# Performance work log

Measured on AMD Instinct MI355X. Metric: run time of the kernel, lower is better.

Reference implementation:

```python
import jax, jax.numpy as jnp
import numpy as np

EPS = 1e-6
INV_T = 1.0
STEPS = 6  # TRAIN_STEPS (module defaults to training mode)
NORM_EPS = 1e-12  # F.normalize default eps


def _l2norm_dim1(t):
    # F.normalize(t, p=2, dim=1): divide by clamped L2 norm over feature dim D
    n = jnp.sqrt(jnp.sum(t * t, axis=1, keepdims=True))
    return t / jnp.maximum(n, NORM_EPS)


def setup_inputs() -> dict:
    key = jax.random.key(0)
    k1, k2 = jax.random.split(key)
    x5d = jax.random.normal(k1, (2, 512, 16, 64, 64), dtype=jnp.float32)
    bases = jax.random.uniform(k2, (2, 512, 64), dtype=jnp.float32)  # (B*S, D_feat, R)
    return {"x5d": x5d, "bases": bases}


def reference(x5d, bases):
    B, C, Dv, H, W = x5d.shape
    S = 1
    D_feat = C // S
    N = Dv * H * W
    x = x5d.reshape(B * S, D_feat, N)  # (BS, D, N)

    b = _l2norm_dim1(bases)  # _build_bases normalizes over D
    # coef init uses UNCLAMPED x (clamp happens in-place only inside local_step)
    coef = jax.nn.softmax(INV_T * jnp.einsum('bdn,bdr->bnr', x, b), axis=-1)

    xc = jnp.maximum(x, EPS)  # clamp_input_nonneg, applied in-place on first MU step

    def mu_step(carry, _):
        b, c = carry
        BtB = jnp.einsum('bdr,bds->brs', b, b)            # (BS,R,R)
        numC = jnp.einsum('bdn,bdr->bnr', xc, b)          # (BS,N,R)
        denC = jnp.einsum('bnr,brs->bns', c, BtB) + EPS
        c = c * numC / denC
        CtC = jnp.einsum('bnr,bns->brs', c, c)            # (BS,R,R)
        numB = jnp.einsum('bdn,bnr->bdr', xc, c)          # (BS,D,R)
        denB = jnp.einsum('bdr,brs->bds', b, CtC) + EPS
        b = b * numB / denB
        b = jnp.maximum(b, EPS)
        c = jnp.maximum(c, EPS)
        b = _l2norm_dim1(b)  # normalize_each_step
        return (b, c), None

    (b, coef), _ = jax.lax.scan(mu_step, (b, coef), None, length=STEPS)

    # compute_coef (differentiable refinement in the original)
    BtB = jnp.einsum('bdr,bds->brs', b, b)
    numC = jnp.einsum('bdn,bdr->bnr', xc, b)
    denC = jnp.einsum('bnr,brs->bns', coef, BtB) + EPS
    c_new = coef * (numC / denC)

    x_hat = jnp.einsum('bdr,bnr->bdn', b, c_new)  # (BS, D, N)
    return x_hat.reshape(B, C, Dv, H, W)
```

## Files before the change

### kernel.cpp

```cpp
#include <hip/hip_runtime.h>
#include <math.h>

#define DD   512
#define NTOT 65536
#define RR   64
#define NB   2
#define EPSV 1e-6f

typedef unsigned short u16;
typedef __attribute__((ext_vector_type(8))) short bf16x8;
typedef __attribute__((ext_vector_type(8))) unsigned short us8;
typedef __attribute__((ext_vector_type(4))) unsigned short us4;
typedef __attribute__((ext_vector_type(4))) float f32x4;

__device__ inline u16 f2bf(float f) {
    union { float f; unsigned u; } x; x.f = f;
    unsigned r = x.u + 0x7FFFu + ((x.u >> 16) & 1u);
    return (u16)(r >> 16);
}
__device__ inline float bf2f(u16 h) {
    union { unsigned u; float f; } x; x.u = ((unsigned)h) << 16;
    return x.f;
}
__device__ inline u16 clamp1(u16 h) {
    short t = (short)h;
    return (u16)(t < (short)0x3586 ? (short)0x3586 : t);
}

#define MFMA16(a, b, c) __builtin_amdgcn_mfma_f32_16x16x32_bf16((a), (b), (c), 0, 0, 0)

__global__ __launch_bounds__(256) void convert_x_kernel(const float* __restrict__ x,
                                                        u16* __restrict__ xd,
                                                        u16* __restrict__ xTr,
                                                        u16* __restrict__ xTc) {
    int s = blockIdx.z, d0 = blockIdx.y * 64, n0 = blockIdx.x * 64;
    const float* xp = x + ((size_t)s * DD + d0) * NTOT + n0;
    u16* xdp = xd + ((size_t)s * DD + d0) * NTOT + n0;
    u16* xtr = xTr + ((size_t)s * NTOT + n0) * DD + d0;
    u16* xtc = xTc + ((size_t)s * NTOT + n0) * DD + d0;
    __shared__ u16 L[64][66];
    int tid = threadIdx.x;
#pragma unroll
    for (int k = 0; k < 4; ++k) {
        int f4 = tid + k * 256;
        int dr = f4 >> 4, c4 = (f4 & 15) * 4;
        float4 v = *(const float4*)&xp[(size_t)dr * NTOT + c4];
        u16 h0 = f2bf(v.x), h1 = f2bf(v.y), h2 = f2bf(v.z), h3 = f2bf(v.w);
        xdp[(size_t)dr * NTOT + c4 + 0] = clamp1(h0);
        xdp[(size_t)dr * NTOT + c4 + 1] = clamp1(h1);
        xdp[(size_t)dr * NTOT + c4 + 2] = clamp1(h2);
        xdp[(size_t)dr * NTOT + c4 + 3] = clamp1(h3);
        L[dr][c4 + 0] = h0; L[dr][c4 + 1] = h1;
        L[dr][c4 + 2] = h2; L[dr][c4 + 3] = h3;
    }
    __syncthreads();
#pragma unroll
    for (int k = 0; k < 2; ++k) {
        int f8 = tid + k * 256;
        int nr = f8 >> 3, d8 = (f8 & 7) * 8;
        us8 wr, wc;
#pragma unroll
        for (int i = 0; i < 8; ++i) {
            u16 h = L[d8 + i][nr];
            wr[i] = h;
            wc[i] = clamp1(h);
        }
        *(us8*)&xtr[(size_t)nr * DD + d8] = wr;
        *(us8*)&xtc[(size_t)nr * DD + d8] = wc;
    }
}

__global__ __launch_bounds__(1024) void bnorm_kernel(const float* __restrict__ src,
                                                     float* __restrict__ b0,
                                                     u16* __restrict__ b_bf,
                                                     u16* __restrict__ bT_bf,
                                                     u16* __restrict__ btb_bf) {
    int s = blockIdx.x, tid = threadIdx.x;
    int r = tid & 63, grp = tid >> 6;
    const float* sp = src + (size_t)s * DD * RR;
    float* b0p = b0 + (size_t)s * DD * RR;
    u16* bbp = b_bf + (size_t)s * DD * RR;
    __shared__ float part[16][64];
    __shared__ float invl[64];
    __shared__ __align__(16) u16 btl[64][520];
    float vv[32];
    float p = 0.f;
#pragma unroll
    for (int i = 0; i < 32; ++i) {
        vv[i] = sp[(grp * 32 + i) * 64 + r];
        p += vv[i] * vv[i];
    }
    part[grp][r] = p;
    __syncthreads();
    if (tid < 64) {
        float ss = 0.f;
#pragma unroll
        for (int k = 0; k < 16; ++k) ss += part[k][tid];
        invl[tid] = 1.f / fmaxf(sqrtf(ss), 1e-12f);
    }
    __syncthreads();
    float inv = invl[r];
#pragma unroll
    for (int i = 0; i < 32; ++i) {
        int d = grp * 32 + i;
        float v = vv[i] * inv;
        b0p[d * 64 + r] = v;
        u16 h = f2bf(v);
        bbp[d * 64 + r] = h;
        btl[r][d] = h;
    }
    __syncthreads();
    u16* btg = bT_bf + (size_t)s * RR * DD;
#pragma unroll
    for (int k = 0; k < 4; ++k) {
        int f8 = tid + k * 1024;
        int row = f8 >> 6, c8 = (f8 & 63) * 8;
        *(us8*)&btg[row * DD + c8] = *(const us8*)&btl[row][c8];
    }
    if (grp < 4) {
        int g = r >> 4, l15 = r & 15;
        f32x4 zero = {0.f, 0.f, 0.f, 0.f};
        f32x4 acc[4];
#pragma unroll
        for (int cs = 0; cs < 4; ++cs) acc[cs] = zero;
        for (int k0 = 0; k0 < DD; k0 += 32) {
            bf16x8 a = *(const bf16x8*)&btl[grp * 16 + l15][k0 + g * 8];
            bf16x8 b[4];
#pragma unroll
            for (int cs = 0; cs < 4; ++cs)
                b[cs] = *(const bf16x8*)&btl[cs * 16 + l15][k0 + g * 8];
#pragma unroll
            for (int cs = 0; cs < 4; ++cs) acc[cs] = MFMA16(a, b[cs], acc[cs]);
        }
        u16* op = btb_bf + (size_t)s * RR * RR;
#pragma unroll
        for (int cs = 0; cs < 4; ++cs)
#pragma unroll
            for (int e = 0; e < 4; ++e)
                op[(grp * 16 + g * 4 + e) * RR + cs * 16 + l15] = f2bf(acc[cs][e]);
    }
}

__global__ __launch_bounds__(256) void init_mfma_kernel(const u16* __restrict__ xT,
                                                        const u16* __restrict__ bT,
                                                        u16* __restrict__ cT,
                                                        u16* __restrict__ cnb) {
    int s = blockIdx.y;
    int n0 = blockIdx.x * 128;
    int tid = threadIdx.x;
    int w = tid >> 6, lane = tid & 63, g = lane >> 4, l15 = lane & 15;
    int nw = n0 + w * 32;
    const u16* xTp = xT + (size_t)s * NTOT * DD;
    const u16* bTp = bT + (size_t)s * RR * DD;
    u16* cTp = cT + (size_t)s * RR * NTOT;
    u16* cnp = cnb + (size_t)s * NTOT * RR;

    f32x4 zero = {0.f, 0.f, 0.f, 0.f};
    f32x4 acc[4][2];
#pragma unroll
    for (int rs = 0; rs < 4; ++rs)
#pragma unroll
        for (int ns = 0; ns < 2; ++ns) acc[rs][ns] = zero;

    bf16x8 aA[4], bA[2], aB[4], bB[2];
#pragma unroll
    for (int rs = 0; rs < 4; ++rs)
        aA[rs] = *(const bf16x8*)&bTp[(rs * 16 + l15) * DD + g * 8];
#pragma unroll
    for (int ns = 0; ns < 2; ++ns)
        bA[ns] = *(const bf16x8*)&xTp[(size_t)(nw + ns * 16 + l15) * DD + g * 8];
#pragma unroll
    for (int i = 0; i < 8; ++i) {
        int kB = i * 64 + 32;
#pragma unroll
        for (int rs = 0; rs < 4; ++rs)
            aB[rs] = *(const bf16x8*)&bTp[(rs * 16 + l15) * DD + kB + g * 8];
#pragma unroll
        for (int ns = 0; ns < 2; ++ns)
            bB[ns] = *(const bf16x8*)&xTp[(size_t)(nw + ns * 16 + l15) * DD + kB + g * 8];
#pragma unroll
        for (int rs = 0; rs < 4; ++rs)
#pragma unroll
            for (int ns = 0; ns < 2; ++ns)
                acc[rs][ns] = MFMA16(aA[rs], bA[ns], acc[rs][ns]);
        int kA = (i < 7) ? i * 64 + 64 : i * 64;
#pragma unroll
        for (int rs = 0; rs < 4; ++rs)
            aA[rs] = *(const bf16x8*)&bTp[(rs * 16 + l15) * DD + kA + g * 8];
#pragma unroll
        for (int ns = 0; ns < 2; ++ns)
            bA[ns] = *(const bf16x8*)&xTp[(size_t)(nw + ns * 16 + l15) * DD + kA + g * 8];
#pragma unroll
        for (int rs = 0; rs < 4; ++rs)
#pragma unroll
            for (int ns = 0; ns < 2; ++ns)
                acc[rs][ns] = MFMA16(aB[rs], bB[ns], acc[rs][ns]);
    }

#pragma unroll
    for (int ns = 0; ns < 2; ++ns) {
        int n = nw + ns * 16 + l15;
        float m = acc[0][ns][0];
#pragma unroll
        for (int rs = 0; rs < 4; ++rs)
#pragma unroll
            for (int e = 0; e < 4; ++e) m = fmaxf(m, acc[rs][ns][e]);
        m = fmaxf(m, __shfl_xor(m, 16));
        m = fmaxf(m, __shfl_xor(m, 32));
        float ev[4][4];
        float ssum = 0.f;
#pragma unroll
        for (int rs = 0; rs < 4; ++rs)
#pragma unroll
            for (int e = 0; e < 4; ++e) {
                ev[rs][e] = __expf(acc[rs][ns][e] - m);
                ssum += ev[rs][e];
            }
        ssum += __shfl_xor(ssum, 16);
        ssum += __shfl_xor(ssum, 32);
        float inv = 1.f / ssum;
#pragma unroll
        for (int rs = 0; rs < 4; ++rs) {
            us4 pack;
#pragma unroll
            for (int e = 0; e < 4; ++e) {
                u16 h = f2bf(ev[rs][e] * inv);
                cTp[(size_t)(rs * 16 + g * 4 + e) * NTOT + n] = h;
                pack[e] = h;
            }
            *(us4*)&cnp[(size_t)n * RR + rs * 16 + g * 4] = pack;
        }
    }
}

template <int CLAMPC>
__global__ __launch_bounds__(256) void xtb_mfma_kernel(const u16* __restrict__ xT,
                                                       const u16* __restrict__ bT,
                                                       const u16* __restrict__ btbbf,
                                                       u16* __restrict__ cnb,
                                                       u16* __restrict__ cT) {
    int s = blockIdx.y;
    int n0 = blockIdx.x * 128;
    int tid = threadIdx.x;
    int w = tid >> 6, lane = tid & 63, g = lane >> 4, l15 = lane & 15;
    int nw = n0 + w * 32;
    const u16* xTp = xT + (size_t)s * NTOT * DD;
    const u16* bTp = bT + (size_t)s * RR * DD;
    const u16* bb = btbbf + (size_t)s * RR * RR;
    u16* cnp = cnb + (size_t)s * NTOT * RR;
    u16* cTp = cT + (size_t)s * RR * NTOT;

    f32x4 zero = {0.f, 0.f, 0.f, 0.f};
    f32x4 accD[4][2], accT[4][2];
#pragma unroll
    for (int rs = 0; rs < 4; ++rs)
#pragma unroll
        for (int ns = 0; ns < 2; ++ns) { accD[rs][ns] = zero; accT[rs][ns] = zero; }

#pragma unroll
    for (int k0 = 0; k0 < 64; k0 += 32) {
        bf16x8 a[4], b[2];
#pragma unroll
        for (int rs = 0; rs < 4; ++rs)
            a[rs] = *(const bf16x8*)&bb[(rs * 16 + l15) * RR + k0 + g * 8];
#pragma unroll
        for (int ns = 0; ns < 2; ++ns)
            b[ns] = *(const bf16x8*)&cnp[(size_t)(nw + ns * 16 + l15) * RR + k0 + g * 8];
#pragma unroll
        for (int rs = 0; rs < 4; ++rs)
#pragma unroll
            for (int ns = 0; ns < 2; ++ns)
                accD[rs][ns] = MFMA16(a[rs], b[ns], accD[rs][ns]);
    }

    {
        bf16x8 aA[4], bA[2], aB[4], bB[2];
#pragma unroll
        for (int rs = 0; rs < 4; ++rs)
            aA[rs] = *(const bf16x8*)&bTp[(rs * 16 + l15) * DD + g * 8];
#pragma unroll
        for (int ns = 0; ns < 2; ++ns)
            bA[ns] = *(const bf16x8*)&xTp[(size_t)(nw + ns * 16 + l15) * DD + g * 8];
#pragma unroll
        for (int i = 0; i < 8; ++i) {
            int kB = i * 64 + 32;
#pragma unroll
            for (int rs = 0; rs < 4; ++rs)
                aB[rs] = *(const bf16x8*)&bTp[(rs * 16 + l15) * DD + kB + g * 8];
#pragma unroll
            for (int ns = 0; ns < 2; ++ns)
                bB[ns] = *(const bf16x8*)&xTp[(size_t)(nw + ns * 16 + l15) * DD + kB + g * 8];
#pragma unroll
            for (int rs = 0; rs < 4; ++rs)
#pragma unroll
                for (int ns = 0; ns < 2; ++ns)
                    accT[rs][ns] = MFMA16(aA[rs], bA[ns], accT[rs][ns]);
            int kA = (i < 7) ? i * 64 + 64 : i * 64;
#pragma unroll
            for (int rs = 0; rs < 4; ++rs)
                aA[rs] = *(const bf16x8*)&bTp[(rs * 16 + l15) * DD + kA + g * 8];
#pragma unroll
            for (int ns = 0; ns < 2; ++ns)
                bA[ns] = *(const bf16x8*)&xTp[(size_t)(nw + ns * 16 + l15) * DD + kA + g * 8];
#pragma unroll
            for (int rs = 0; rs < 4; ++rs)
#pragma unroll
                for (int ns = 0; ns < 2; ++ns)
                    accT[rs][ns] = MFMA16(aB[rs], bB[ns], accT[rs][ns]);
        }
    }

#pragma unroll
    for (int ns = 0; ns < 2; ++ns) {
        int n = nw + ns * 16 + l15;
#pragma unroll
        for (int rs = 0; rs < 4; ++rs) {
            us4 pack;
#pragma unroll
            for (int e = 0; e < 4; ++e) {
                int r = rs * 16 + g * 4 + e;
                size_t off = (size_t)r * NTOT + n;
                float cin = bf2f(cTp[off]);
                if (CLAMPC) cin = fmaxf(cin, EPSV);
                float v = cin * accT[rs][ns][e] / (accD[rs][ns][e] + EPSV);
                u16 h = f2bf(v);
                cTp[off] = h;
                pack[e] = clamp1(h);
            }
            *(us4*)&cnp[(size_t)n * RR + rs * 16 + g * 4] = pack;
        }
    }
}

__global__ __launch_bounds__(256) void ctc_mfma_kernel(const u16* __restrict__ cT,
                                                       float* __restrict__ ctc) {
    int s = blockIdx.y;
    int kbase = blockIdx.x * 512;
    int tid = threadIdx.x;
    int w = tid >> 6, lane = tid & 63, g = lane >> 4, l15 = lane & 15;
    const u16* cTp = cT + (size_t)s * RR * NTOT;
    const u16* arow = cTp + (size_t)(w * 16 + l15) * NTOT;
    f32x4 zero = {0.f, 0.f, 0.f, 0.f};
    f32x4 acc[4];
#pragma unroll
    for (int cs = 0; cs < 4; ++cs) acc[cs] = zero;

    bf16x8 aA, bA[4], aB, bB[4];
    aA = *(const bf16x8*)&arow[kbase + g * 8];
#pragma unroll
    for (int cs = 0; cs < 4; ++cs)
        bA[cs] = *(const bf16x8*)&cTp[(size_t)(cs * 16 + l15) * NTOT + kbase + g * 8];
#pragma unroll
    for (int i = 0; i < 8; ++i) {
        int kB = kbase + i * 64 + 32;
        aB = *(const bf16x8*)&arow[kB + g * 8];
#pragma unroll
        for (int cs = 0; cs < 4; ++cs)
            bB[cs] = *(const bf16x8*)&cTp[(size_t)(cs * 16 + l15) * NTOT + kB + g * 8];
#pragma unroll
        for (int cs = 0; cs < 4; ++cs) acc[cs] = MFMA16(aA, bA[cs], acc[cs]);
        int kA = (i < 7) ? kbase + i * 64 + 64 : kbase;
        aA = *(const bf16x8*)&arow[kA + g * 8];
#pragma unroll
        for (int cs = 0; cs < 4; ++cs)
            bA[cs] = *(const bf16x8*)&cTp[(size_t)(cs * 16 + l15) * NTOT + kA + g * 8];
#pragma unroll
        for (int cs = 0; cs < 4; ++cs) acc[cs] = MFMA16(aB, bB[cs], acc[cs]);
    }
    float* op = ctc + (size_t)s * RR * RR;
#pragma unroll
    for (int cs = 0; cs < 4; ++cs)
#pragma unroll
        for (int e = 0; e < 4; ++e)
            atomicAdd(&op[(w * 16 + g * 4 + e) * RR + cs * 16 + l15], acc[cs][e]);
}

__global__ __launch_bounds__(256) void xtc_mfma_kernel(const u16* __restrict__ xd,
                                                       const u16* __restrict__ cT,
                                                       float* __restrict__ numB) {
    int s = blockIdx.z;
    int dtile = blockIdx.y * 64;
    int kbase = blockIdx.x * 2048;
    int tid = threadIdx.x;
    int w = tid >> 6, lane = tid & 63, g = lane >> 4, l15 = lane & 15;
    const u16* arow = xd + (size_t)s * DD * NTOT + (size_t)(dtile + w * 16 + l15) * NTOT;
    const u16* cTp = cT + (size_t)s * RR * NTOT;
    f32x4 zero = {0.f, 0.f, 0.f, 0.f};
    f32x4 acc[4];
#pragma unroll
    for (int rs = 0; rs < 4; ++rs) acc[rs] = zero;

    bf16x8 aA, bA[4], aB, bB[4];
    aA = *(const bf16x8*)&arow[kbase + g * 8];
#pragma unroll
    for (int rs = 0; rs < 4; ++rs)
        bA[rs] = *(const bf16x8*)&cTp[(size_t)(rs * 16 + l15) * NTOT + kbase + g * 8];
#pragma unroll
    for (int i = 0; i < 32; ++i) {
        int kB = kbase + i * 64 + 32;
        aB = *(const bf16x8*)&arow[kB + g * 8];
#pragma unroll
        for (int rs = 0; rs < 4; ++rs)
            bB[rs] = *(const bf16x8*)&cTp[(size_t)(rs * 16 + l15) * NTOT + kB + g * 8];
#pragma unroll
        for (int rs = 0; rs < 4; ++rs) acc[rs] = MFMA16(aA, bA[rs], acc[rs]);
        int kA = (i < 31) ? kbase + i * 64 + 64 : kbase;
        aA = *(const bf16x8*)&arow[kA + g * 8];
#pragma unroll
        for (int rs = 0; rs < 4; ++rs)
            bA[rs] = *(const bf16x8*)&cTp[(size_t)(rs * 16 + l15) * NTOT + kA + g * 8];
#pragma unroll
        for (int rs = 0; rs < 4; ++rs) acc[rs] = MFMA16(aB, bB[rs], acc[rs]);
    }
    float* op = numB + (size_t)s * DD * RR;
#pragma unroll
    for (int rs = 0; rs < 4; ++rs)
#pragma unroll
        for (int e = 0; e < 4; ++e)
            atomicAdd(&op[(dtile + w * 16 + g * 4 + e) * RR + rs * 16 + l15], acc[rs][e]);
}

__global__ __launch_bounds__(256) void bupd_s_kernel(float* __restrict__ b0,
                                                     const float* __restrict__ numB,
                                                     const float* __restrict__ ctcG) {
    int s = blockIdx.y;
    int d0 = blockIdx.x * 64;
    float* bp = b0 + ((size_t)s * DD + d0) * RR;
    const float* np_ = numB + ((size_t)s * DD + d0) * RR;
    const float* cc = ctcG + (size_t)s * RR * RR;
    __shared__ __align__(16) float Bsh[64][68];
    __shared__ __align__(16) float Ct[64][68];
    int tid = threadIdx.x, tx = tid & 15, ty = tid >> 4;
#pragma unroll
    for (int k = 0; k < 16; ++k) {
        int idx = tid + k * 256;
        int r_ = idx >> 6, col = idx & 63;
        Bsh[r_][col] = bp[idx];
        Ct[r_][col] = cc[idx];
    }
    __syncthreads();
#pragma unroll
    for (int i = 0; i < 4; ++i) {
        int d = 4 * ty + i;
        float den[4] = {};
#pragma unroll
        for (int k = 0; k < 64; ++k) {
            float bv = Bsh[d][k];
            float4 ct = *(const float4*)&Ct[k][4 * tx];
            den[0] += bv * ct.x;
            den[1] += bv * ct.y;
            den[2] += bv * ct.z;
            den[3] += bv * ct.w;
        }
        float4 b4 = *(const float4*)&Bsh[d][4 * tx];
        float4 n4 = *(const float4*)&np_[(size_t)d * RR + 4 * tx];
        float4 o;
        o.x = fmaxf(b4.x * n4.x / (den[0] + EPSV), EPSV);
        o.y = fmaxf(b4.y * n4.y / (den[1] + EPSV), EPSV);
        o.z = fmaxf(b4.z * n4.z / (den[2] + EPSV), EPSV);
        o.w = fmaxf(b4.w * n4.w / (den[3] + EPSV), EPSV);
        *(float4*)&bp[(size_t)d * RR + 4 * tx] = o;
    }
}

__global__ __launch_bounds__(256) void cfinal_kernel(const u16* __restrict__ xT,
                                                     const u16* __restrict__ bT,
                                                     const u16* __restrict__ btbbf,
                                                     const u16* __restrict__ cnb,
                                                     const u16* __restrict__ cT,
                                                     const u16* __restrict__ b_bf,
                                                     float* __restrict__ outp) {
    int s = blockIdx.y;
    int n0 = blockIdx.x * 128;
    int tid = threadIdx.x;
    int w = tid >> 6, lane = tid & 63, g = lane >> 4, l15 = lane & 15;
    int nw = n0 + w * 32;
    const u16* xTp = xT + (size_t)s * NTOT * DD;
    const u16* bTp = bT + (size_t)s * RR * DD;
    const u16* bb = btbbf + (size_t)s * RR * RR;
    const u16* cnp = cnb + (size_t)s * NTOT * RR;
    const u16* cTp = cT + (size_t)s * RR * NTOT;
    __shared__ __align__(16) u16 CL[128][72];

    f32x4 zero = {0.f, 0.f, 0.f, 0.f};
    f32x4 accD[4][2], accT[4][2];
#pragma unroll
    for (int rs = 0; rs < 4; ++rs)
#pragma unroll
        for (int ns = 0; ns < 2; ++ns) { accD[rs][ns] = zero; accT[rs][ns] = zero; }

#pragma unroll
    for (int k0 = 0; k0 < 64; k0 += 32) {
        bf16x8 a[4], b[2];
#pragma unroll
        for (int rs = 0; rs < 4; ++rs)
            a[rs] = *(const bf16x8*)&bb[(rs * 16 + l15) * RR + k0 + g * 8];
#pragma unroll
        for (int ns = 0; ns < 2; ++ns)
            b[ns] = *(const bf16x8*)&cnp[(size_t)(nw + ns * 16 + l15) * RR + k0 + g * 8];
#pragma unroll
        for (int rs = 0; rs < 4; ++rs)
#pragma unroll
            for (int ns = 0; ns < 2; ++ns)
                accD[rs][ns] = MFMA16(a[rs], b[ns], accD[rs][ns]);
    }
    {
        bf16x8 aA[4], bA[2], aB[4], bB[2];
#pragma unroll
        for (int rs = 0; rs < 4; ++rs)
            aA[rs] = *(const bf16x8*)&bTp[(rs * 16 + l15) * DD + g * 8];
#pragma unroll
        for (int ns = 0; ns < 2; ++ns)
            bA[ns] = *(const bf16x8*)&xTp[(size_t)(nw + ns * 16 + l15) * DD + g * 8];
#pragma unroll
        for (int i = 0; i < 8; ++i) {
            int kB = i * 64 + 32;
#pragma unroll
            for (int rs = 0; rs < 4; ++rs)
                aB[rs] = *(const bf16x8*)&bTp[(rs * 16 + l15) * DD + kB + g * 8];
#pragma unroll
            for (int ns = 0; ns < 2; ++ns)
                bB[ns] = *(const bf16x8*)&xTp[(size_t)(nw + ns * 16 + l15) * DD + kB + g * 8];
#pragma unroll
            for (int rs = 0; rs < 4; ++rs)
#pragma unroll
                for (int ns = 0; ns < 2; ++ns)
                    accT[rs][ns] = MFMA16(aA[rs], bA[ns], accT[rs][ns]);
            int kA = (i < 7) ? i * 64 + 64 : i * 64;
#pragma unroll
            for (int rs = 0; rs < 4; ++rs)
                aA[rs] = *(const bf16x8*)&bTp[(rs * 16 + l15) * DD + kA + g * 8];
#pragma unroll
            for (int ns = 0; ns < 2; ++ns)
                bA[ns] = *(const bf16x8*)&xTp[(size_t)(nw + ns * 16 + l15) * DD + kA + g * 8];
#pragma unroll
            for (int rs = 0; rs < 4; ++rs)
#pragma unroll
                for (int ns = 0; ns < 2; ++ns)
                    accT[rs][ns] = MFMA16(aB[rs], bB[ns], accT[rs][ns]);
        }
    }
#pragma unroll
    for (int ns = 0; ns < 2; ++ns) {
        int n = nw + ns * 16 + l15;
        int nloc = w * 32 + ns * 16 + l15;
#pragma unroll
        for (int rs = 0; rs < 4; ++rs) {
            us4 pack;
#pragma unroll
            for (int e = 0; e < 4; ++e) {
                int r = rs * 16 + g * 4 + e;
                float cin = fmaxf(bf2f(cTp[(size_t)r * NTOT + n]), EPSV);
                float v = cin * accT[rs][ns][e] / (accD[rs][ns][e] + EPSV);
                pack[e] = f2bf(v);
            }
            *(us4*)&CL[nloc][rs * 16 + g * 4] = pack;
        }
    }
    __syncthreads();
    bf16x8 bf_[8][2];
#pragma unroll
    for (int nf = 0; nf < 8; ++nf)
#pragma unroll
        for (int kc = 0; kc < 2; ++kc)
            bf_[nf][kc] = *(const bf16x8*)&CL[nf * 16 + l15][kc * 32 + g * 8];
    const u16* bbp = b_bf + (size_t)s * DD * RR;
    float* op = outp + (size_t)s * DD * NTOT;
#pragma unroll
    for (int df = 0; df < 8; ++df) {
        int d = w * 128 + df * 16 + l15;
        bf16x8 a0 = *(const bf16x8*)&bbp[d * RR + g * 8];
        bf16x8 a1 = *(const bf16x8*)&bbp[d * RR + 32 + g * 8];
        f32x4 acc[8];
#pragma unroll
        for (int nf = 0; nf < 8; ++nf) acc[nf] = zero;
#pragma unroll
        for (int nf = 0; nf < 8; ++nf) {
            acc[nf] = MFMA16(a0, bf_[nf][0], acc[nf]);
            acc[nf] = MFMA16(a1, bf_[nf][1], acc[nf]);
        }
#pragma unroll
        for (int nf = 0; nf < 8; ++nf)
#pragma unroll
            for (int e = 0; e < 4; ++e)
                op[(size_t)(w * 128 + df * 16 + g * 4 + e) * NTOT + n0 + nf * 16 + l15] =
                    acc[nf][e];
    }
}

extern "C" void kernel_launch(void* const* d_in, const int* in_sizes, int n_in,
                              void* d_out, int out_size, void* d_ws, size_t ws_size,
                              hipStream_t stream) {
    const float* x = (const float*)d_in[0];
    const float* bases = (const float*)d_in[1];
    float* out = (float*)d_out;
    char* ws = (char*)d_ws;

    u16* cTf = (u16*)ws;
    u16* cnb = (u16*)(ws + 16777216);
    u16* xTc = (u16*)(ws + 33554432);
    u16* xTr = (u16*)(ws + 167772160);
    u16* xd  = (u16*)(ws + 301989888);
    float* b0 = (float*)(ws + 436207616);
    float* ctc = (float*)(ws + 436469760);
    float* nB = (float*)(ws + 436502528);
    u16* b_bf = (u16*)(ws + 436764672);
    u16* bT_bf = (u16*)(ws + 436895744);
    u16* btb_bf = (u16*)(ws + 437026816);

    convert_x_kernel<<<dim3(NTOT / 64, DD / 64, NB), 256, 0, stream>>>(x, xd, xTr, xTc);

    bnorm_kernel<<<NB, 1024, 0, stream>>>(bases, b0, b_bf, bT_bf, btb_bf);

    init_mfma_kernel<<<dim3(NTOT / 128, NB), 256, 0, stream>>>(xTr, bT_bf, cTf, cnb);

    for (int step = 0; step < 6; ++step) {
        if (step > 0)
            xtb_mfma_kernel<1><<<dim3(NTOT / 128, NB), 256, 0, stream>>>(
                xTc, bT_bf, btb_bf, cnb, cTf);
        else
            xtb_mfma_kernel<0><<<dim3(NTOT / 128, NB), 256, 0, stream>>>(
                xTc, bT_bf, btb_bf, cnb, cTf);
        hipMemsetAsync(ctc, 0, 32768 + 262144, stream);
        ctc_mfma_kernel<<<dim3(128, NB), 256, 0, stream>>>(cTf, ctc);
        xtc_mfma_kernel<<<dim3(32, 8, NB), 256, 0, stream>>>(xd, cTf, nB);
        bupd_s_kernel<<<dim3(8, NB), 256, 0, stream>>>(b0, nB, ctc);
        bnorm_kernel<<<NB, 1024, 0, stream>>>(b0, b0, b_bf, bT_bf, btb_bf);
    }

    cfinal_kernel<<<dim3(NTOT / 128, NB), 256, 0, stream>>>(
        xTc, bT_bf, btb_bf, cnb, cTf, b_bf, out);
}
```

Measured before the change: 1.466 ms.

## Fuse CtC into xtc kernel, zero accumulators in bnorm, vectorize convert stores

```diff
diff --git a/kernel.cpp b/kernel.cpp
--- a/kernel.cpp
+++ b/kernel.cpp
@@ -38,7 +38,7 @@
     u16* xdp = xd + ((size_t)s * DD + d0) * NTOT + n0;
     u16* xtr = xTr + ((size_t)s * NTOT + n0) * DD + d0;
     u16* xtc = xTc + ((size_t)s * NTOT + n0) * DD + d0;
-    __shared__ u16 L[64][66];
+    __shared__ __align__(16) u16 L[64][72];
     int tid = threadIdx.x;
 #pragma unroll
     for (int k = 0; k < 4; ++k) {
@@ -46,12 +46,12 @@
         int dr = f4 >> 4, c4 = (f4 & 15) * 4;
         float4 v = *(const float4*)&xp[(size_t)dr * NTOT + c4];
         u16 h0 = f2bf(v.x), h1 = f2bf(v.y), h2 = f2bf(v.z), h3 = f2bf(v.w);
-        xdp[(size_t)dr * NTOT + c4 + 0] = clamp1(h0);
-        xdp[(size_t)dr * NTOT + c4 + 1] = clamp1(h1);
-        xdp[(size_t)dr * NTOT + c4 + 2] = clamp1(h2);
-        xdp[(size_t)dr * NTOT + c4 + 3] = clamp1(h3);
-        L[dr][c4 + 0] = h0; L[dr][c4 + 1] = h1;
-        L[dr][c4 + 2] = h2; L[dr][c4 + 3] = h3;
+        us4 pc;
+        pc[0] = clamp1(h0); pc[1] = clamp1(h1);
+        pc[2] = clamp1(h2); pc[3] = clamp1(h3);
+        *(us4*)&xdp[(size_t)dr * NTOT + c4] = pc;
+        us4 pr; pr[0] = h0; pr[1] = h1; pr[2] = h2; pr[3] = h3;
+        *(us4*)&L[dr][c4] = pr;
     }
     __syncthreads();
 #pragma unroll
@@ -74,12 +74,23 @@
                                                      float* __restrict__ b0,
                                                      u16* __restrict__ b_bf,
                                                      u16* __restrict__ bT_bf,
-                                                     u16* __restrict__ btb_bf) {
+                                                     u16* __restrict__ btb_bf,
+                                                     float* __restrict__ ctcZ,
+                                                     float* __restrict__ nBZ) {
     int s = blockIdx.x, tid = threadIdx.x;
     int r = tid & 63, grp = tid >> 6;
     const float* sp = src + (size_t)s * DD * RR;
     float* b0p = b0 + (size_t)s * DD * RR;
     u16* bbp = b_bf + (size_t)s * DD * RR;
+    {
+        float4 z4 = {0.f, 0.f, 0.f, 0.f};
+        float* zc = ctcZ + (size_t)s * RR * RR;
+        float* zn = nBZ + (size_t)s * DD * RR;
+        *(float4*)&zc[tid * 4] = z4;
+#pragma unroll
+        for (int k = 0; k < 8; ++k)
+            *(float4*)&zn[(tid + k * 1024) * 4] = z4;
+    }
     __shared__ float part[16][64];
     __shared__ float invl[64];
     __shared__ __align__(16) u16 btl[64][520];
@@ -332,69 +343,38 @@
     }
 }
 
-__global__ __launch_bounds__(256) void ctc_mfma_kernel(const u16* __restrict__ cT,
-                                                       float* __restrict__ ctc) {
-    int s = blockIdx.y;
-    int kbase = blockIdx.x * 512;
-    int tid = threadIdx.x;
-    int w = tid >> 6, lane = tid & 63, g = lane >> 4, l15 = lane & 15;
-    const u16* cTp = cT + (size_t)s * RR * NTOT;
-    const u16* arow = cTp + (size_t)(w * 16 + l15) * NTOT;
-    f32x4 zero = {0.f, 0.f, 0.f, 0.f};
-    f32x4 acc[4];
-#pragma unroll
-    for (int cs = 0; cs < 4; ++cs) acc[cs] = zero;
-
-    bf16x8 aA, bA[4], aB, bB[4];
-    aA = *(const bf16x8*)&arow[kbase + g * 8];
-#pragma unroll
-    for (int cs = 0; cs < 4; ++cs)
-        bA[cs] = *(const bf16x8*)&cTp[(size_t)(cs * 16 + l15) * NTOT + kbase + g * 8];
-#pragma unroll
-    for (int i = 0; i < 8; ++i) {
-        int kB = kbase + i * 64 + 32;
-        aB = *(const bf16x8*)&arow[kB + g * 8];
-#pragma unroll
-        for (int cs = 0; cs < 4; ++cs)
-            bB[cs] = *(const bf16x8*)&cTp[(size_t)(cs * 16 + l15) * NTOT + kB + g * 8];
-#pragma unroll
-        for (int cs = 0; cs < 4; ++cs) acc[cs] = MFMA16(aA, bA[cs], acc[cs]);
-        int kA = (i < 7) ? kbase + i * 64 + 64 : kbase;
-        aA = *(const bf16x8*)&arow[kA + g * 8];
-#pragma unroll
-        for (int cs = 0; cs < 4; ++cs)
-            bA[cs] = *(const bf16x8*)&cTp[(size_t)(cs * 16 + l15) * NTOT + kA + g * 8];
-#pragma unroll
-        for (int cs = 0; cs < 4; ++cs) acc[cs] = MFMA16(aB, bB[cs], acc[cs]);
-    }
-    float* op = ctc + (size_t)s * RR * RR;
-#pragma unroll
-    for (int cs = 0; cs < 4; ++cs)
-#pragma unroll
-        for (int e = 0; e < 4; ++e)
-            atomicAdd(&op[(w * 16 + g * 4 + e) * RR + cs * 16 + l15], acc[cs][e]);
-}
-
-__global__ __launch_bounds__(256) void xtc_mfma_kernel(const u16* __restrict__ xd,
-                                                       const u16* __restrict__ cT,
-                                                       float* __restrict__ numB) {
+__global__ __launch_bounds__(256) void xtc_ctc_kernel(const u16* __restrict__ xd,
+                                                      const u16* __restrict__ cT,
+                                                      float* __restrict__ numB,
+                                                      float* __restrict__ ctc) {
     int s = blockIdx.z;
-    int dtile = blockIdx.y * 64;
+    int dt = blockIdx.y;
+    int dtile = dt * 64;
     int kbase = blockIdx.x * 2048;
     int tid = threadIdx.x;
     int w = tid >> 6, lane = tid & 63, g = lane >> 4, l15 = lane & 15;
     const u16* arow = xd + (size_t)s * DD * NTOT + (size_t)(dtile + w * 16 + l15) * NTOT;
     const u16* cTp = cT + (size_t)s * RR * NTOT;
+    int ii = dt >> 1;
+    int jj = (dt & 1) * 2;
+    const u16* cRowI = cTp + (size_t)(ii * 16 + l15) * NTOT;
+    const u16* cRowJ0 = cTp + (size_t)(jj * 16 + l15) * NTOT;
+    const u16* cRowJ1 = cTp + (size_t)((jj + 1) * 16 + l15) * NTOT;
+
     f32x4 zero = {0.f, 0.f, 0.f, 0.f};
-    f32x4 acc[4];
+    f32x4 acc[4], accC0 = zero, accC1 = zero;
 #pragma unroll
     for (int rs = 0; rs < 4; ++rs) acc[rs] = zero;
 
     bf16x8 aA, bA[4], aB, bB[4];
+    bf16x8 cIa, cJ0a, cJ1a, cIb, cJ0b, cJ1b;
     aA = *(const bf16x8*)&arow[kbase + g * 8];
 #pragma unroll
     for (int rs = 0; rs < 4; ++rs)
         bA[rs] = *(const bf16x8*)&cTp[(size_t)(rs * 16 + l15) * NTOT + kbase + g * 8];
+    cIa = *(const bf16x8*)&cRowI[kbase + g * 8];
+    cJ0a = *(const bf16x8*)&cRowJ0[kbase + g * 8];
+    cJ1a = *(const bf16x8*)&cRowJ1[kbase + g * 8];
 #pragma unroll
     for (int i = 0; i < 32; ++i) {
         int kB = kbase + i * 64 + 32;
@@ -402,15 +382,25 @@
 #pragma unroll
         for (int rs = 0; rs < 4; ++rs)
             bB[rs] = *(const bf16x8*)&cTp[(size_t)(rs * 16 + l15) * NTOT + kB + g * 8];
+        cIb = *(const bf16x8*)&cRowI[kB + g * 8];
+        cJ0b = *(const bf16x8*)&cRowJ0[kB + g * 8];
+        cJ1b = *(const bf16x8*)&cRowJ1[kB + g * 8];
 #pragma unroll
         for (int rs = 0; rs < 4; ++rs) acc[rs] = MFMA16(aA, bA[rs], acc[rs]);
+        accC0 = MFMA16(cIa, cJ0a, accC0);
+        accC1 = MFMA16(cIa, cJ1a, accC1);
         int kA = (i < 31) ? kbase + i * 64 + 64 : kbase;
         aA = *(const bf16x8*)&arow[kA + g * 8];
 #pragma unroll
         for (int rs = 0; rs < 4; ++rs)
             bA[rs] = *(const bf16x8*)&cTp[(size_t)(rs * 16 + l15) * NTOT + kA + g * 8];
+        cIa = *(const bf16x8*)&cRowI[kA + g * 8];
+        cJ0a = *(const bf16x8*)&cRowJ0[kA + g * 8];
+        cJ1a = *(const bf16x8*)&cRowJ1[kA + g * 8];
 #pragma unroll
         for (int rs = 0; rs < 4; ++rs) acc[rs] = MFMA16(aB, bB[rs], acc[rs]);
+        accC0 = MFMA16(cIb, cJ0b, accC0);
+        accC1 = MFMA16(cIb, cJ1b, accC1);
     }
     float* op = numB + (size_t)s * DD * RR;
 #pragma unroll
@@ -418,6 +408,12 @@
 #pragma unroll
         for (int e = 0; e < 4; ++e)
             atomicAdd(&op[(dtile + w * 16 + g * 4 + e) * RR + rs * 16 + l15], acc[rs][e]);
+    float* cp = ctc + (size_t)s * RR * RR;
+#pragma unroll
+    for (int e = 0; e < 4; ++e) {
+        atomicAdd(&cp[(ii * 16 + g * 4 + e) * RR + jj * 16 + l15], accC0[e]);
+        atomicAdd(&cp[(ii * 16 + g * 4 + e) * RR + (jj + 1) * 16 + l15], accC1[e]);
+    }
 }
 
 __global__ __launch_bounds__(256) void bupd_s_kernel(float* __restrict__ b0,
@@ -610,7 +606,7 @@
 
     convert_x_kernel<<<dim3(NTOT / 64, DD / 64, NB), 256, 0, stream>>>(x, xd, xTr, xTc);
 
-    bnorm_kernel<<<NB, 1024, 0, stream>>>(bases, b0, b_bf, bT_bf, btb_bf);
+    bnorm_kernel<<<NB, 1024, 0, stream>>>(bases, b0, b_bf, bT_bf, btb_bf, ctc, nB);
 
     init_mfma_kernel<<<dim3(NTOT / 128, NB), 256, 0, stream>>>(xTr, bT_bf, cTf, cnb);
 
@@ -621,11 +617,9 @@
         else
             xtb_mfma_kernel<0><<<dim3(NTOT / 128, NB), 256, 0, stream>>>(
                 xTc, bT_bf, btb_bf, cnb, cTf);
-        hipMemsetAsync(ctc, 0, 32768 + 262144, stream);
-        ctc_mfma_kernel<<<dim3(128, NB), 256, 0, stream>>>(cTf, ctc);
-        xtc_mfma_kernel<<<dim3(32, 8, NB), 256, 0, stream>>>(xd, cTf, nB);
+        xtc_ctc_kernel<<<dim3(32, 8, NB), 256, 0, stream>>>(xd, cTf, nB, ctc);
         bupd_s_kernel<<<dim3(8, NB), 256, 0, stream>>>(b0, nB, ctc);
-        bnorm_kernel<<<NB, 1024, 0, stream>>>(b0, b0, b_bf, bT_bf, btb_bf);
+        bnorm_kernel<<<NB, 1024, 0, stream>>>(b0, b0, b_bf, bT_bf, btb_bf, ctc, nB);
     }
 
     cfinal_kernel<<<dim3(NTOT / 128, NB), 256, 0, stream>>>(
```

Result: slower. 1.644 ms (+12.2%).

## Fuse CtC computation into coef update and clamp x on the fly

Applied to the files above, without the earlier changes.

```diff
diff --git a/kernel.cpp b/kernel.cpp
--- a/kernel.cpp
+++ b/kernel.cpp
@@ -26,18 +26,24 @@
     short t = (short)h;
     return (u16)(t < (short)0x3586 ? (short)0x3586 : t);
 }
+__device__ inline bf16x8 clampbf8(bf16x8 v) {
+#pragma unroll
+    for (int i = 0; i < 8; ++i) {
+        short t = v[i];
+        v[i] = (t < (short)0x3586) ? (short)0x3586 : t;
+    }
+    return v;
+}
 
 #define MFMA16(a, b, c) __builtin_amdgcn_mfma_f32_16x16x32_bf16((a), (b), (c), 0, 0, 0)
 
 __global__ __launch_bounds__(256) void convert_x_kernel(const float* __restrict__ x,
                                                         u16* __restrict__ xd,
-                                                        u16* __restrict__ xTr,
-                                                        u16* __restrict__ xTc) {
+                                                        u16* __restrict__ xTr) {
     int s = blockIdx.z, d0 = blockIdx.y * 64, n0 = blockIdx.x * 64;
     const float* xp = x + ((size_t)s * DD + d0) * NTOT + n0;
     u16* xdp = xd + ((size_t)s * DD + d0) * NTOT + n0;
     u16* xtr = xTr + ((size_t)s * NTOT + n0) * DD + d0;
-    u16* xtc = xTc + ((size_t)s * NTOT + n0) * DD + d0;
     __shared__ u16 L[64][66];
     int tid = threadIdx.x;
 #pragma unroll
@@ -58,15 +64,10 @@
     for (int k = 0; k < 2; ++k) {
         int f8 = tid + k * 256;
         int nr = f8 >> 3, d8 = (f8 & 7) * 8;
-        us8 wr, wc;
-#pragma unroll
-        for (int i = 0; i < 8; ++i) {
-            u16 h = L[d8 + i][nr];
-            wr[i] = h;
-            wc[i] = clamp1(h);
-        }
+        us8 wr;
+#pragma unroll
+        for (int i = 0; i < 8; ++i) wr[i] = L[d8 + i][nr];
         *(us8*)&xtr[(size_t)nr * DD + d8] = wr;
-        *(us8*)&xtc[(size_t)nr * DD + d8] = wc;
     }
 }
 
@@ -238,7 +239,8 @@
                                                        const u16* __restrict__ bT,
                                                        const u16* __restrict__ btbbf,
                                                        u16* __restrict__ cnb,
-                                                       u16* __restrict__ cT) {
+                                                       u16* __restrict__ cT,
+                                                       float* __restrict__ ctc) {
     int s = blockIdx.y;
     int n0 = blockIdx.x * 128;
     int tid = threadIdx.x;
@@ -249,6 +251,7 @@
     const u16* bb = btbbf + (size_t)s * RR * RR;
     u16* cnp = cnb + (size_t)s * NTOT * RR;
     u16* cTp = cT + (size_t)s * RR * NTOT;
+    __shared__ __align__(16) u16 T[64][132];
 
     f32x4 zero = {0.f, 0.f, 0.f, 0.f};
     f32x4 accD[4][2], accT[4][2];
@@ -280,7 +283,7 @@
             aA[rs] = *(const bf16x8*)&bTp[(rs * 16 + l15) * DD + g * 8];
 #pragma unroll
         for (int ns = 0; ns < 2; ++ns)
-            bA[ns] = *(const bf16x8*)&xTp[(size_t)(nw + ns * 16 + l15) * DD + g * 8];
+            bA[ns] = clampbf8(*(const bf16x8*)&xTp[(size_t)(nw + ns * 16 + l15) * DD + g * 8]);
 #pragma unroll
         for (int i = 0; i < 8; ++i) {
             int kB = i * 64 + 32;
@@ -289,7 +292,7 @@
                 aB[rs] = *(const bf16x8*)&bTp[(rs * 16 + l15) * DD + kB + g * 8];
 #pragma unroll
             for (int ns = 0; ns < 2; ++ns)
-                bB[ns] = *(const bf16x8*)&xTp[(size_t)(nw + ns * 16 + l15) * DD + kB + g * 8];
+                bB[ns] = clampbf8(*(const bf16x8*)&xTp[(size_t)(nw + ns * 16 + l15) * DD + kB + g * 8]);
 #pragma unroll
             for (int rs = 0; rs < 4; ++rs)
 #pragma unroll
@@ -301,7 +304,7 @@
                 aA[rs] = *(const bf16x8*)&bTp[(rs * 16 + l15) * DD + kA + g * 8];
 #pragma unroll
             for (int ns = 0; ns < 2; ++ns)
-                bA[ns] = *(const bf16x8*)&xTp[(size_t)(nw + ns * 16 + l15) * DD + kA + g * 8];
+                bA[ns] = clampbf8(*(const bf16x8*)&xTp[(size_t)(nw + ns * 16 + l15) * DD + kA + g * 8]);
 #pragma unroll
             for (int rs = 0; rs < 4; ++rs)
 #pragma unroll
@@ -313,6 +316,7 @@
 #pragma unroll
     for (int ns = 0; ns < 2; ++ns) {
         int n = nw + ns * 16 + l15;
+        int nloc = w * 32 + ns * 16 + l15;
 #pragma unroll
         for (int rs = 0; rs < 4; ++rs) {
             us4 pack;
@@ -325,54 +329,31 @@
                 float v = cin * accT[rs][ns][e] / (accD[rs][ns][e] + EPSV);
                 u16 h = f2bf(v);
                 cTp[off] = h;
+                T[r][nloc] = h;
                 pack[e] = clamp1(h);
             }
             *(us4*)&cnp[(size_t)n * RR + rs * 16 + g * 4] = pack;
         }
     }
-}
-
-__global__ __launch_bounds__(256) void ctc_mfma_kernel(const u16* __restrict__ cT,
-                                                       float* __restrict__ ctc) {
-    int s = blockIdx.y;
-    int kbase = blockIdx.x * 512;
-    int tid = threadIdx.x;
-    int w = tid >> 6, lane = tid & 63, g = lane >> 4, l15 = lane & 15;
-    const u16* cTp = cT + (size_t)s * RR * NTOT;
-    const u16* arow = cTp + (size_t)(w * 16 + l15) * NTOT;
-    f32x4 zero = {0.f, 0.f, 0.f, 0.f};
-    f32x4 acc[4];
-#pragma unroll
-    for (int cs = 0; cs < 4; ++cs) acc[cs] = zero;
-
-    bf16x8 aA, bA[4], aB, bB[4];
-    aA = *(const bf16x8*)&arow[kbase + g * 8];
-#pragma unroll
-    for (int cs = 0; cs < 4; ++cs)
-        bA[cs] = *(const bf16x8*)&cTp[(size_t)(cs * 16 + l15) * NTOT + kbase + g * 8];
-#pragma unroll
-    for (int i = 0; i < 8; ++i) {
-        int kB = kbase + i * 64 + 32;
-        aB = *(const bf16x8*)&arow[kB + g * 8];
-#pragma unroll
-        for (int cs = 0; cs < 4; ++cs)
-            bB[cs] = *(const bf16x8*)&cTp[(size_t)(cs * 16 + l15) * NTOT + kB + g * 8];
-#pragma unroll
-        for (int cs = 0; cs < 4; ++cs) acc[cs] = MFMA16(aA, bA[cs], acc[cs]);
-        int kA = (i < 7) ? kbase + i * 64 + 64 : kbase;
-        aA = *(const bf16x8*)&arow[kA + g * 8];
-#pragma unroll
-        for (int cs = 0; cs < 4; ++cs)
-            bA[cs] = *(const bf16x8*)&cTp[(size_t)(cs * 16 + l15) * NTOT + kA + g * 8];
-#pragma unroll
-        for (int cs = 0; cs < 4; ++cs) acc[cs] = MFMA16(aB, bB[cs], acc[cs]);
-    }
-    float* op = ctc + (size_t)s * RR * RR;
-#pragma unroll
-    for (int cs = 0; cs < 4; ++cs)
-#pragma unroll
-        for (int e = 0; e < 4; ++e)
-            atomicAdd(&op[(w * 16 + g * 4 + e) * RR + cs * 16 + l15], acc[cs][e]);
+    __syncthreads();
+
+    {
+        int k0 = w * 32;
+        bf16x8 fr[4];
+#pragma unroll
+        for (int i = 0; i < 4; ++i)
+            fr[i] = *(const bf16x8*)&T[i * 16 + l15][k0 + g * 8];
+        float* cp = ctc + (size_t)s * RR * RR;
+#pragma unroll
+        for (int i = 0; i < 4; ++i)
+#pragma unroll
+            for (int j = 0; j < 4; ++j) {
+                f32x4 cc = MFMA16(fr[i], fr[j], zero);
+#pragma unroll
+                for (int e = 0; e < 4; ++e)
+                    atomicAdd(&cp[(i * 16 + g * 4 + e) * RR + j * 16 + l15], cc[e]);
+            }
+    }
 }
 
 __global__ __launch_bounds__(256) void xtc_mfma_kernel(const u16* __restrict__ xd,
@@ -511,7 +492,7 @@
             aA[rs] = *(const bf16x8*)&bTp[(rs * 16 + l15) * DD + g * 8];
 #pragma unroll
         for (int ns = 0; ns < 2; ++ns)
-            bA[ns] = *(const bf16x8*)&xTp[(size_t)(nw + ns * 16 + l15) * DD + g * 8];
+            bA[ns] = clampbf8(*(const bf16x8*)&xTp[(size_t)(nw + ns * 16 + l15) * DD + g * 8]);
 #pragma unroll
         for (int i = 0; i < 8; ++i) {
             int kB = i * 64 + 32;
@@ -520,7 +501,7 @@
                 aB[rs] = *(const bf16x8*)&bTp[(rs * 16 + l15) * DD + kB + g * 8];
 #pragma unroll
             for (int ns = 0; ns < 2; ++ns)
-                bB[ns] = *(const bf16x8*)&xTp[(size_t)(nw + ns * 16 + l15) * DD + kB + g * 8];
+                bB[ns] = clampbf8(*(const bf16x8*)&xTp[(size_t)(nw + ns * 16 + l15) * DD + kB + g * 8]);
 #pragma unroll
             for (int rs = 0; rs < 4; ++rs)
 #pragma unroll
@@ -532,7 +513,7 @@
                 aA[rs] = *(const bf16x8*)&bTp[(rs * 16 + l15) * DD + kA + g * 8];
 #pragma unroll
             for (int ns = 0; ns < 2; ++ns)
-                bA[ns] = *(const bf16x8*)&xTp[(size_t)(nw + ns * 16 + l15) * DD + kA + g * 8];
+                bA[ns] = clampbf8(*(const bf16x8*)&xTp[(size_t)(nw + ns * 16 + l15) * DD + kA + g * 8]);
 #pragma unroll
             for (int rs = 0; rs < 4; ++rs)
 #pragma unroll
@@ -598,36 +579,34 @@
 
     u16* cTf = (u16*)ws;
     u16* cnb = (u16*)(ws + 16777216);
-    u16* xTc = (u16*)(ws + 33554432);
-    u16* xTr = (u16*)(ws + 167772160);
-    u16* xd  = (u16*)(ws + 301989888);
-    float* b0 = (float*)(ws + 436207616);
-    float* ctc = (float*)(ws + 436469760);
-    float* nB = (float*)(ws + 436502528);
-    u16* b_bf = (u16*)(ws + 436764672);
-    u16* bT_bf = (u16*)(ws + 436895744);
-    u16* btb_bf = (u16*)(ws + 437026816);
-
-    convert_x_kernel<<<dim3(NTOT / 64, DD / 64, NB), 256, 0, stream>>>(x, xd, xTr, xTc);
+    u16* xTr = (u16*)(ws + 33554432);
+    u16* xd  = (u16*)(ws + 167772160);
+    float* b0 = (float*)(ws + 301989888);
+    float* ctc = (float*)(ws + 302252032);
+    float* nB = (float*)(ws + 302284800);
+    u16* b_bf = (u16*)(ws + 302546944);
+    u16* bT_bf = (u16*)(ws + 302678016);
+    u16* btb_bf = (u16*)(ws + 302809088);
+
+    convert_x_kernel<<<dim3(NTOT / 64, DD / 64, NB), 256, 0, stream>>>(x, xd, xTr);
 
     bnorm_kernel<<<NB, 1024, 0, stream>>>(bases, b0, b_bf, bT_bf, btb_bf);
 
     init_mfma_kernel<<<dim3(NTOT / 128, NB), 256, 0, stream>>>(xTr, bT_bf, cTf, cnb);
 
     for (int step = 0; step < 6; ++step) {
+        hipMemsetAsync(ctc, 0, 32768 + 262144, stream);
         if (step > 0)
             xtb_mfma_kernel<1><<<dim3(NTOT / 128, NB), 256, 0, stream>>>(
-                xTc, bT_bf, btb_bf, cnb, cTf);
+                xTr, bT_bf, btb_bf, cnb, cTf, ctc);
         else
             xtb_mfma_kernel<0><<<dim3(NTOT / 128, NB), 256, 0, stream>>>(
-                xTc, bT_bf, btb_bf, cnb, cTf);
-        hipMemsetAsync(ctc, 0, 32768 + 262144, stream);
-        ctc_mfma_kernel<<<dim3(128, NB), 256, 0, stream>>>(cTf, ctc);
+                xTr, bT_bf, btb_bf, cnb, cTf, ctc);
         xtc_mfma_kernel<<<dim3(32, 8, NB), 256, 0, stream>>>(xd, cTf, nB);
         bupd_s_kernel<<<dim3(8, NB), 256, 0, stream>>>(b0, nB, ctc);
         bnorm_kernel<<<NB, 1024, 0, stream>>>(b0, b0, b_bf, bT_bf, btb_bf);
     }
 
     cfinal_kernel<<<dim3(NTOT / 128, NB), 256, 0, stream>>>(
-        xTc, bT_bf, btb_bf, cnb, cTf, b_bf, out);
-}
+        xTr, bT_bf, btb_bf, cnb, cTf, b_bf, out);
+}
```

Measured after the change: 1.968 ms. 34.2% more time.
